# Optimization experiments

Hardware: AMD Instinct MI355X
Metric: run time of the kernel (lower is better)

## Reference

```python
import jax, jax.numpy as jnp
import numpy as np

N_NODES = 100000


def _graph_conv(x, W, b, src, dst, inv_sqrt_out, inv_sqrt_in):
    # DGL GraphConv, norm='both':  D_in^{-1/2} A D_out^{-1/2} X W + b
    h = x * inv_sqrt_out[:, None]
    if W.shape[0] > W.shape[1]:
        # in_feats > out_feats: transform first (cheaper aggregation)
        h = h @ W
        m = jax.ops.segment_sum(h[src], dst, num_segments=N_NODES)
    else:
        m = jax.ops.segment_sum(h[src], dst, num_segments=N_NODES)
        m = m @ W
    return m * inv_sqrt_in[:, None] + b


def _degree_norms(src, dst):
    ones = jnp.ones(src.shape[0], dtype=jnp.float32)
    out_deg = jax.ops.segment_sum(ones, src, num_segments=N_NODES)
    in_deg = jax.ops.segment_sum(ones, dst, num_segments=N_NODES)
    # DGL clamps degree to min 1 (allow_zero_in_degree)
    return jnp.clip(out_deg, 1.0) ** -0.5, jnp.clip(in_deg, 1.0) ** -0.5


def setup_inputs() -> dict:
    key = jax.random.key(0)
    ks = jax.random.split(key, 8)
    E = 800000
    in_feats, h1, h2, nc = 128, 256, 128, 40
    return {
        "features": jax.random.normal(ks[0], (N_NODES, in_feats), dtype=jnp.float32),
        "src": jax.random.randint(ks[1], (E,), 0, N_NODES),
        "dst": jax.random.randint(ks[2], (E,), 0, N_NODES),
        "W1": jax.random.normal(ks[3], (in_feats, h1), dtype=jnp.float32) * (2.0 / (in_feats + h1)) ** 0.5,
        "b1": jnp.zeros((h1,), dtype=jnp.float32),
        "W2": jax.random.normal(ks[4], (h1, h2), dtype=jnp.float32) * (2.0 / (h1 + h2)) ** 0.5,
        "b2": jnp.zeros((h2,), dtype=jnp.float32),
        "W3": jax.random.normal(ks[5], (h2, nc), dtype=jnp.float32) * (2.0 / (h2 + nc)) ** 0.5,
        "b3": jnp.zeros((nc,), dtype=jnp.float32),
    }


def reference(features, src, dst, W1, b1, W2, b2, W3, b3):
    inv_out, inv_in = _degree_norms(src, dst)
    h = _graph_conv(features, W1, b1, src, dst, inv_out, inv_in)
    h = jax.nn.relu(h)
    h = _graph_conv(h, W2, b2, src, dst, inv_out, inv_in)
    h = jax.nn.relu(h)
    return _graph_conv(h, W3, b3, src, dst, inv_out, inv_in)
```

## Files before the change

kernel.cpp:

```cpp
#include <hip/hip_runtime.h>

#define N_NODES 100000
#define SCAN_NB 128
#define SCAN_TPB 256

typedef _Float16 half_t;
typedef __attribute__((ext_vector_type(8))) _Float16 v8h;
typedef __attribute__((ext_vector_type(4))) _Float16 v4h;
typedef __attribute__((ext_vector_type(4))) float v4f;


__global__ void prep1(const int* __restrict__ src, const int* __restrict__ dst,
                      int* __restrict__ ocnt, int* __restrict__ icnt, int E,
                      const float* __restrict__ W1, const float* __restrict__ W2,
                      const float* __restrict__ W3, half_t* __restrict__ Wt1,
                      half_t* __restrict__ Wt2, half_t* __restrict__ Wt3) {
    int t = blockIdx.x * blockDim.x + threadIdx.x;
    if (t < E) {
        atomicAdd(&ocnt[src[t]], 1);
        atomicAdd(&icnt[dst[t]], 1);
    } else {
        int u = t - E;
        if (u < 32768) {
            int n = u >> 7, k = u & 127;
            Wt1[u] = (half_t)W1[(size_t)k * 256 + n];
        } else if (u < 65536) {
            int w = u - 32768;
            int n = w >> 8, k = w & 255;
            Wt2[w] = (half_t)W2[(size_t)k * 128 + n];
        } else if (u < 70656) {
            int w = u - 65536;
            int n = w >> 7, k = w & 127;
            Wt3[w] = (half_t)W3[(size_t)k * 40 + n];
        }
    }
}


__global__ __launch_bounds__(SCAN_TPB) void scan_reduce(const int* __restrict__ cnt,
                                                        int* __restrict__ blockSum, int n) {
    __shared__ int s[SCAN_TPB];
    int chunk = (n + SCAN_NB - 1) / SCAN_NB;
    int beg = blockIdx.x * chunk;
    int end = min(beg + chunk, n);
    int sum = 0;
    for (int i = beg + threadIdx.x; i < end; i += SCAN_TPB) sum += cnt[i];
    s[threadIdx.x] = sum;
    __syncthreads();
    for (int off = SCAN_TPB / 2; off > 0; off >>= 1) {
        if (threadIdx.x < off) s[threadIdx.x] += s[threadIdx.x + off];
        __syncthreads();
    }
    if (threadIdx.x == 0) blockSum[blockIdx.x] = s[0];
}

__global__ __launch_bounds__(SCAN_NB) void scan_offsets(int* __restrict__ blockSum,
                                                        int* __restrict__ rowptr_total) {
    __shared__ int s[SCAN_NB];
    int tid = threadIdx.x;
    int v = blockSum[tid];
    s[tid] = v;
    __syncthreads();
    for (int off = 1; off < SCAN_NB; off <<= 1) {
        int t = (tid >= off) ? s[tid - off] : 0;
        __syncthreads();
        s[tid] += t;
        __syncthreads();
    }
    blockSum[tid] = s[tid] - v;
    if (tid == SCAN_NB - 1) rowptr_total[0] = s[tid];
}

__global__ __launch_bounds__(SCAN_TPB) void scan_final(int* __restrict__ cnt,
                                                       int* __restrict__ ocnt,
                                                       const int* __restrict__ blockSum,
                                                       int* __restrict__ rowptr,
                                                       int* __restrict__ cursor, int n) {
    __shared__ int s[SCAN_TPB];
    int chunk = (n + SCAN_NB - 1) / SCAN_NB;
    int beg = blockIdx.x * chunk;
    int end = min(beg + chunk, n);
    int carry = blockSum[blockIdx.x];
    for (int base = beg; base < end; base += SCAN_TPB) {
        int i = base + threadIdx.x;
        int v = (i < end) ? cnt[i] : 0;
        s[threadIdx.x] = v;
        __syncthreads();
        for (int off = 1; off < SCAN_TPB; off <<= 1) {
            int t = (threadIdx.x >= off) ? s[threadIdx.x - off] : 0;
            __syncthreads();
            s[threadIdx.x] += t;
            __syncthreads();
        }
        int excl = s[threadIdx.x] - v;
        if (i < end) {
            rowptr[i] = carry + excl;
            cursor[i] = carry + excl;
            int o = ocnt[i];
            ((float*)ocnt)[i] = rsqrtf((float)max(o, 1));
            ((float*)cnt)[i] = rsqrtf((float)max(v, 1));
        }
        int roundSum = s[SCAN_TPB - 1];
        __syncthreads();
        carry += roundSum;
    }
}


__global__ void prep2(const int* __restrict__ src, const int* __restrict__ dst,
                      int* __restrict__ cursor, int* __restrict__ eidx, int E,
                      const float* __restrict__ x, const float* __restrict__ invOut,
                      half_t* __restrict__ xh) {
    int t = blockIdx.x * blockDim.x + threadIdx.x;
    if (t < E) {
        int pos = atomicAdd(&cursor[dst[t]], 1);
        eidx[pos] = src[t];
    } else {
        int u = t - E;
        if (u < N_NODES * 32) {
            int n = u >> 5;
            float4 v = ((const float4*)x)[u];
            float s = invOut[n];
            v4h h;
            h[0] = (half_t)(v.x * s);
            h[1] = (half_t)(v.y * s);
            h[2] = (half_t)(v.z * s);
            h[3] = (half_t)(v.w * s);
            *(v4h*)(xh + (size_t)u * 4) = h;
        }
    }
}


template <int F>
__device__ __forceinline__ void gather_row(const half_t* __restrict__ x,
                                           const int* __restrict__ eidx,
                                           int beg, int end, int c, float* acc) {
    const half_t* __restrict__ xc = x + (size_t)c * 8;
    int n = end - beg;
    int nb = n & ~3;
    int j = 0;
    if (nb) {
        int i0 = eidx[beg + 0], i1 = eidx[beg + 1], i2 = eidx[beg + 2], i3 = eidx[beg + 3];
        do {
            v8h v0 = *(const v8h*)(xc + (size_t)i0 * F);
            v8h v1 = *(const v8h*)(xc + (size_t)i1 * F);
            v8h v2 = *(const v8h*)(xc + (size_t)i2 * F);
            v8h v3 = *(const v8h*)(xc + (size_t)i3 * F);
            j += 4;
            if (j < nb) {
                i0 = eidx[beg + j + 0];
                i1 = eidx[beg + j + 1];
                i2 = eidx[beg + j + 2];
                i3 = eidx[beg + j + 3];
            }
#pragma unroll
            for (int q = 0; q < 8; ++q)
                acc[q] += ((float)v0[q] + (float)v1[q]) + ((float)v2[q] + (float)v3[q]);
        } while (j < nb);
    }
    for (; j < n; ++j) {
        int s = eidx[beg + j];
        v8h val = *(const v8h*)(xc + (size_t)s * F);
#pragma unroll
        for (int q = 0; q < 8; ++q) acc[q] += (float)val[q];
    }
}


__global__ __launch_bounds__(512) void fused_l12(
    const half_t* __restrict__ xh, const int* __restrict__ rowptr,
    const int* __restrict__ eidx, const half_t* __restrict__ Wt1,
    const half_t* __restrict__ Wt2,
    const float* __restrict__ invIn, const float* __restrict__ invOut,
    const float* __restrict__ b1, half_t* __restrict__ t2) {
    constexpr int K1 = 128, K2 = 256, N2 = 128;
    constexpr int LDA = K1 + 8;
    constexpr int LDH = K2 + 8;
    __shared__ half_t As[64][LDA];
    __shared__ half_t h1S[64][LDH];
    __shared__ float iiS[64], ioS[64];
    const int tid = threadIdx.x;
    const int wave = tid >> 6, lane = tid & 63;
    const int quad = lane >> 4, l16 = lane & 15;
    const int m0 = blockIdx.x * 64;
    const int n0 = wave * 32;

    v8h b[2][4];
    float bv[2];
#pragma unroll
    for (int j = 0; j < 2; ++j) {
        int gn = n0 + j * 16 + l16;
        bv[j] = b1[gn];
#pragma unroll
        for (int kc = 0; kc < 4; ++kc)
            b[j][kc] = *(const v8h*)(Wt1 + (size_t)gn * K1 + kc * 32 + quad * 8);
    }
    if (tid < 64) {
        int gm = m0 + tid;
        bool ok = gm < N_NODES;
        iiS[tid] = ok ? invIn[gm] : 0.f;
        ioS[tid] = ok ? invOut[gm] : 0.f;
    }

#pragma unroll
    for (int t = 0; t < 2; ++t) {
        int task = tid + t * 512;
        int r = task >> 4, c = task & 15;
        int gm = m0 + r;
        float acc[8] = {};
        if (gm < N_NODES)
            gather_row<K1>(xh, eidx, rowptr[gm], rowptr[gm + 1], c, acc);
        v8h o;
#pragma unroll
        for (int q = 0; q < 8; ++q) o[q] = (half_t)acc[q];
        *(v8h*)&As[r][c * 8] = o;
    }
    __syncthreads();

    for (int mt = 0; mt < 4; ++mt) {
        v8h a[4];
#pragma unroll
        for (int kc = 0; kc < 4; ++kc)
            a[kc] = *(const v8h*)&As[mt * 16 + l16][kc * 32 + quad * 8];
        v4f acc[2] = {};
#pragma unroll
        for (int kc = 0; kc < 4; ++kc)
#pragma unroll
            for (int j = 0; j < 2; ++j)
                acc[j] = __builtin_amdgcn_mfma_f32_16x16x32_f16(a[kc], b[j][kc], acc[j], 0, 0, 0);
#pragma unroll
        for (int j = 0; j < 2; ++j) {
            int cn = n0 + j * 16 + l16;
#pragma unroll
            for (int r = 0; r < 4; ++r) {
                int lr = mt * 16 + quad * 4 + r;
                float z = (acc[j][r] * iiS[lr] + bv[j]) * ioS[lr];
                h1S[lr][cn] = (half_t)fmaxf(z, 0.f);
            }
        }
    }

    v8h b2[8];
    const int n02 = wave * 16;
    {
        int gn = n02 + l16;
#pragma unroll
        for (int kc = 0; kc < 8; ++kc)
            b2[kc] = *(const v8h*)(Wt2 + (size_t)gn * K2 + kc * 32 + quad * 8);
    }
    __syncthreads();

    for (int mt = 0; mt < 4; ++mt) {
        v8h a2[8];
#pragma unroll
        for (int kc = 0; kc < 8; ++kc)
            a2[kc] = *(const v8h*)&h1S[mt * 16 + l16][kc * 32 + quad * 8];
        v4f acc2 = {};
#pragma unroll
        for (int kc = 0; kc < 8; ++kc)
            acc2 = __builtin_amdgcn_mfma_f32_16x16x32_f16(a2[kc], b2[kc], acc2, 0, 0, 0);
        int gn = n02 + l16;
#pragma unroll
        for (int r = 0; r < 4; ++r) {
            int gm = m0 + mt * 16 + quad * 4 + r;
            if (gm < N_NODES) t2[(size_t)gm * N2 + gn] = (half_t)acc2[r];
        }
    }
}


__global__ __launch_bounds__(256) void fused_l3(
    const half_t* __restrict__ t2, const int* __restrict__ rowptr,
    const int* __restrict__ eidx, const half_t* __restrict__ Wt3,
    const float* __restrict__ invIn, const float* __restrict__ invOut,
    const float* __restrict__ b2, half_t* __restrict__ t3) {
    constexpr int K = 128, N = 40, LDA = K + 8;
    __shared__ half_t As[64][LDA];
    const int tid = threadIdx.x;
    const int wave = tid >> 6, lane = tid & 63;
    const int quad = lane >> 4, l16 = lane & 15;
    const int m0 = blockIdx.x * 64;

    v8h b[3][4];
#pragma unroll
    for (int j = 0; j < 3; ++j) {
        int gn = j * 16 + l16;
#pragma unroll
        for (int kc = 0; kc < 4; ++kc)
            b[j][kc] = (gn < N) ? *(const v8h*)(Wt3 + (size_t)gn * K + kc * 32 + quad * 8)
                                : (v8h)(half_t)0;
    }

#pragma unroll
    for (int t = 0; t < 4; ++t) {
        int task = tid + t * 256;
        int r = task >> 4, c = task & 15;
        int gm = m0 + r;
        float acc[8] = {};
        float ii = 0.f, io = 0.f;
        if (gm < N_NODES) {
            ii = invIn[gm];
            io = invOut[gm];
            gather_row<K>(t2, eidx, rowptr[gm], rowptr[gm + 1], c, acc);
        }
        v8h o;
#pragma unroll
        for (int q = 0; q < 8; ++q)
            o[q] = (half_t)fmaxf((acc[q] * ii + b2[c * 8 + q]) * io, 0.f);
        *(v8h*)&As[r][c * 8] = o;
    }
    __syncthreads();

    {
        int mt = wave;
        v8h a[4];
#pragma unroll
        for (int kc = 0; kc < 4; ++kc)
            a[kc] = *(const v8h*)&As[mt * 16 + l16][kc * 32 + quad * 8];
        v4f acc[3] = {};
#pragma unroll
        for (int kc = 0; kc < 4; ++kc)
#pragma unroll
            for (int j = 0; j < 3; ++j)
                acc[j] = __builtin_amdgcn_mfma_f32_16x16x32_f16(a[kc], b[j][kc], acc[j], 0, 0, 0);
#pragma unroll
        for (int j = 0; j < 3; ++j) {
            int gn = j * 16 + l16;
            if (gn >= N) continue;
#pragma unroll
            for (int r = 0; r < 4; ++r) {
                int gm = m0 + mt * 16 + quad * 4 + r;
                if (gm < N_NODES) t3[(size_t)gm * N + gn] = (half_t)acc[j][r];
            }
        }
    }
}


__global__ void gather_final(const half_t* __restrict__ x,
                             const int* __restrict__ rowptr, const int* __restrict__ eidx,
                             float* __restrict__ out, const float* __restrict__ invIn,
                             const float* __restrict__ bias) {
    constexpr int F = 40, V = 5;
    int t = blockIdx.x * blockDim.x + threadIdx.x;
    int n = t / V;
    int v = t - n * V;
    if (n >= N_NODES) return;
    float acc[8] = {};
    gather_row<F>(x, eidx, rowptr[n], rowptr[n + 1], v, acc);
    float ii = invIn[n];
    float* o = out + (size_t)n * F + v * 8;
#pragma unroll
    for (int q = 0; q < 8; ++q) o[q] = acc[q] * ii + bias[v * 8 + q];
}


extern "C" void kernel_launch(void* const* d_in, const int* in_sizes, int n_in,
                              void* d_out, int out_size, void* d_ws, size_t ws_size,
                              hipStream_t stream) {
    const float* x  = (const float*)d_in[0];
    const int* src  = (const int*)d_in[1];
    const int* dst  = (const int*)d_in[2];
    const float* W1 = (const float*)d_in[3];
    const float* b1 = (const float*)d_in[4];
    const float* W2 = (const float*)d_in[5];
    const float* b2 = (const float*)d_in[6];
    const float* W3 = (const float*)d_in[7];
    const float* b3 = (const float*)d_in[8];
    float* out = (float*)d_out;
    const int E = in_sizes[1];

    char* ws = (char*)d_ws;
    int* ocnt     = (int*)ws;
    int* icnt     = (int*)(ws + 400000);
    int* rowptr   = (int*)(ws + 800000);
    int* cursor   = (int*)(ws + 1200256);
    int* eidx     = (int*)(ws + 1600256);
    int* blockSum = (int*)(ws + 4800256);
    half_t* Wt1   = (half_t*)(ws + 4800768);
    half_t* Wt2   = (half_t*)(ws + 4866304);
    half_t* Wt3   = (half_t*)(ws + 4931840);
    half_t* buf0  = (half_t*)(ws + 5000192);
    half_t* buf1  = (half_t*)(ws + 30600192);
    const float* inv_out = (const float*)ocnt;
    const float* inv_in  = (const float*)icnt;

    hipMemsetAsync(ocnt, 0, 800000, stream);
    prep1<<<(E + 70656 + 255) / 256, 256, 0, stream>>>(src, dst, ocnt, icnt, E,
                                                       W1, W2, W3, Wt1, Wt2, Wt3);
    scan_reduce<<<SCAN_NB, SCAN_TPB, 0, stream>>>(icnt, blockSum, N_NODES);
    scan_offsets<<<1, SCAN_NB, 0, stream>>>(blockSum, rowptr + N_NODES);
    scan_final<<<SCAN_NB, SCAN_TPB, 0, stream>>>(icnt, ocnt, blockSum, rowptr, cursor, N_NODES);
    prep2<<<(E + N_NODES * 32 + 255) / 256, 256, 0, stream>>>(src, dst, cursor, eidx, E,
                                                              x, inv_out, buf0);

    const int NB = (N_NODES + 63) / 64;

    fused_l12<<<NB, 512, 0, stream>>>(buf0, rowptr, eidx, Wt1, Wt2,
                                      inv_in, inv_out, b1, buf1);
    fused_l3<<<NB, 256, 0, stream>>>(buf1, rowptr, eidx, Wt3, inv_in, inv_out, b2, buf0);
    gather_final<<<(N_NODES * 5 + 255) / 256, 256, 0, stream>>>(
        buf0, rowptr, eidx, out, inv_in, b3);
}
```

Before: 348.5 us.

## Split fused gather+GEMM kernels into standalone gather and MLP kernels

Unfuses the neighbor aggregation from the MFMA matmul kernels. Gathers now run in separate high-occupancy kernels (launch_bounds 256,8) that write aggregated rows to global memory, and the MLP kernels read those rows back. The aim is to keep the latency-bound gathers from being limited by the occupancy of the large-LDS, 512-thread GEMM blocks. The cost is extra global write and read traffic for the intermediate buffers (about 25MB each) and two extra kernel launches.

```diff
diff --git a/kernel.cpp b/kernel.cpp
--- a/kernel.cpp
+++ b/kernel.cpp
@@ -168,9 +168,44 @@
 }
 
 
-__global__ __launch_bounds__(512) void fused_l12(
+__global__ __launch_bounds__(256, 8) void gather1(
     const half_t* __restrict__ xh, const int* __restrict__ rowptr,
-    const int* __restrict__ eidx, const half_t* __restrict__ Wt1,
+    const int* __restrict__ eidx, half_t* __restrict__ A1) {
+    int t = blockIdx.x * 256 + threadIdx.x;
+    int n = t >> 4, c = t & 15;
+    if (n >= N_NODES) return;
+    float acc[8] = {};
+    gather_row<128>(xh, eidx, rowptr[n], rowptr[n + 1], c, acc);
+    v8h o;
+#pragma unroll
+    for (int q = 0; q < 8; ++q) o[q] = (half_t)acc[q];
+    *(v8h*)(A1 + (size_t)n * 128 + c * 8) = o;
+}
+
+__global__ __launch_bounds__(256, 8) void gather2(
+    const half_t* __restrict__ t2, const int* __restrict__ rowptr,
+    const int* __restrict__ eidx, const float* __restrict__ invIn,
+    const float* __restrict__ invOut, const float* __restrict__ b2,
+    half_t* __restrict__ A2) {
+    int t = blockIdx.x * 256 + threadIdx.x;
+    int n = t >> 4, c = t & 15;
+    if (n >= N_NODES) return;
+    float acc[8] = {};
+    gather_row<128>(t2, eidx, rowptr[n], rowptr[n + 1], c, acc);
+    float ii = invIn[n], io = invOut[n];
+    float4 blo = ((const float4*)b2)[c * 2];
+    float4 bhi = ((const float4*)b2)[c * 2 + 1];
+    float bb[8] = {blo.x, blo.y, blo.z, blo.w, bhi.x, bhi.y, bhi.z, bhi.w};
+    v8h o;
+#pragma unroll
+    for (int q = 0; q < 8; ++q)
+        o[q] = (half_t)fmaxf((acc[q] * ii + bb[q]) * io, 0.f);
+    *(v8h*)(A2 + (size_t)n * 128 + c * 8) = o;
+}
+
+
+__global__ __launch_bounds__(512) void mlp12(
+    const half_t* __restrict__ A1, const half_t* __restrict__ Wt1,
     const half_t* __restrict__ Wt2,
     const float* __restrict__ invIn, const float* __restrict__ invOut,
     const float* __restrict__ b1, half_t* __restrict__ t2) {
@@ -204,17 +239,13 @@
     }
 
 #pragma unroll
-    for (int t = 0; t < 2; ++t) {
-        int task = tid + t * 512;
+    for (int p = 0; p < 2; ++p) {
+        int task = tid + p * 512;
         int r = task >> 4, c = task & 15;
         int gm = m0 + r;
-        float acc[8] = {};
-        if (gm < N_NODES)
-            gather_row<K1>(xh, eidx, rowptr[gm], rowptr[gm + 1], c, acc);
-        v8h o;
-#pragma unroll
-        for (int q = 0; q < 8; ++q) o[q] = (half_t)acc[q];
-        *(v8h*)&As[r][c * 8] = o;
+        v8h v = (gm < N_NODES) ? *(const v8h*)(A1 + (size_t)gm * K1 + c * 8)
+                               : (v8h)(half_t)0;
+        *(v8h*)&As[r][c * 8] = v;
     }
     __syncthreads();
 
@@ -270,11 +301,9 @@
 }
 
 
-__global__ __launch_bounds__(256) void fused_l3(
-    const half_t* __restrict__ t2, const int* __restrict__ rowptr,
-    const int* __restrict__ eidx, const half_t* __restrict__ Wt3,
-    const float* __restrict__ invIn, const float* __restrict__ invOut,
-    const float* __restrict__ b2, half_t* __restrict__ t3) {
+__global__ __launch_bounds__(256) void mlp3(
+    const half_t* __restrict__ A2, const half_t* __restrict__ Wt3,
+    half_t* __restrict__ t3) {
     constexpr int K = 128, N = 40, LDA = K + 8;
     __shared__ half_t As[64][LDA];
     const int tid = threadIdx.x;
@@ -293,22 +322,13 @@
     }
 
 #pragma unroll
-    for (int t = 0; t < 4; ++t) {
-        int task = tid + t * 256;
+    for (int p = 0; p < 4; ++p) {
+        int task = tid + p * 256;
         int r = task >> 4, c = task & 15;
         int gm = m0 + r;
-        float acc[8] = {};
-        float ii = 0.f, io = 0.f;
-        if (gm < N_NODES) {
-            ii = invIn[gm];
-            io = invOut[gm];
-            gather_row<K>(t2, eidx, rowptr[gm], rowptr[gm + 1], c, acc);
-        }
-        v8h o;
-#pragma unroll
-        for (int q = 0; q < 8; ++q)
-            o[q] = (half_t)fmaxf((acc[q] * ii + b2[c * 8 + q]) * io, 0.f);
-        *(v8h*)&As[r][c * 8] = o;
+        v8h v = (gm < N_NODES) ? *(const v8h*)(A2 + (size_t)gm * K + c * 8)
+                               : (v8h)(half_t)0;
+        *(v8h*)&As[r][c * 8] = v;
     }
     __syncthreads();
 
@@ -338,10 +358,11 @@
 }
 
 
-__global__ void gather_final(const half_t* __restrict__ x,
-                             const int* __restrict__ rowptr, const int* __restrict__ eidx,
-                             float* __restrict__ out, const float* __restrict__ invIn,
-                             const float* __restrict__ bias) {
+__global__ __launch_bounds__(256, 8) void gather_final(
+    const half_t* __restrict__ x,
+    const int* __restrict__ rowptr, const int* __restrict__ eidx,
+    float* __restrict__ out, const float* __restrict__ invIn,
+    const float* __restrict__ bias) {
     constexpr int F = 40, V = 5;
     int t = blockIdx.x * blockDim.x + threadIdx.x;
     int n = t / V;
@@ -381,8 +402,8 @@
     half_t* Wt1   = (half_t*)(ws + 4800768);
     half_t* Wt2   = (half_t*)(ws + 4866304);
     half_t* Wt3   = (half_t*)(ws + 4931840);
-    half_t* buf0  = (half_t*)(ws + 5000192);
-    half_t* buf1  = (half_t*)(ws + 30600192);
+    half_t* bufA  = (half_t*)(ws + 5000192);
+    half_t* bufB  = (half_t*)(ws + 30600192);
     const float* inv_out = (const float*)ocnt;
     const float* inv_in  = (const float*)icnt;
 
@@ -393,13 +414,15 @@
     scan_offsets<<<1, SCAN_NB, 0, stream>>>(blockSum, rowptr + N_NODES);
     scan_final<<<SCAN_NB, SCAN_TPB, 0, stream>>>(icnt, ocnt, blockSum, rowptr, cursor, N_NODES);
     prep2<<<(E + N_NODES * 32 + 255) / 256, 256, 0, stream>>>(src, dst, cursor, eidx, E,
-                                                              x, inv_out, buf0);
-
-    const int NB = (N_NODES + 63) / 64;
-
-    fused_l12<<<NB, 512, 0, stream>>>(buf0, rowptr, eidx, Wt1, Wt2,
-                                      inv_in, inv_out, b1, buf1);
-    fused_l3<<<NB, 256, 0, stream>>>(buf1, rowptr, eidx, Wt3, inv_in, inv_out, b2, buf0);
+                                                              x, inv_out, bufA);
+
+    const int NBG = (N_NODES * 16 + 255) / 256;
+    const int NB  = (N_NODES + 63) / 64;
+
+    gather1<<<NBG, 256, 0, stream>>>(bufA, rowptr, eidx, bufB);
+    mlp12<<<NB, 512, 0, stream>>>(bufB, Wt1, Wt2, inv_in, inv_out, b1, bufA);
+    gather2<<<NBG, 256, 0, stream>>>(bufA, rowptr, eidx, inv_in, inv_out, b2, bufB);
+    mlp3<<<NB, 256, 0, stream>>>(bufB, Wt3, bufA);
     gather_final<<<(N_NODES * 5 + 255) / 256, 256, 0, stream>>>(
-        buf0, rowptr, eidx, out, inv_in, b3);
-}
+        bufA, rowptr, eidx, out, inv_in, b3);
+}
```

Result: no change. 355.4 us (+2.0%).
